# Kernel tuning notes

Measured on AMD Instinct MI355X. Metric: run time of the kernel, lower is better.

## Reference

```python
import jax, jax.numpy as jnp
import numpy as np

NEG_SLOPE = 0.1

def lrelu(x):
    return jnp.where(x >= 0, x, NEG_SLOPE * x)

def conv2d(x, w, b, padding=0, dilation=1):
    y = jax.lax.conv_general_dilated(
        x, w, window_strides=(1, 1),
        padding=[(padding, padding), (padding, padding)],
        rhs_dilation=(dilation, dilation),
        dimension_numbers=('NCHW', 'OIHW', 'NCHW'))
    return y + b[None, :, None, None]

def res_aspp(x, p):
    r1 = lrelu(conv2d(x, p['a1_w'], p['a1_b'], padding=1, dilation=1))
    r2 = lrelu(conv2d(x, p['a2_w'], p['a2_b'], padding=2, dilation=2))
    r3 = lrelu(conv2d(x, p['a3_w'], p['a3_b'], padding=4, dilation=4))
    r = conv2d(jnp.concatenate((r1, r2, r3), axis=1), p['ar_w'], p['ar_b'])
    return x + r

def deform_conv2d(x, offset, w, b):
    # x: [B,C,H,W], offset: [B,2*K,H,W] torchvision layout (y,x) per 3x3 tap
    B, C, H, W = x.shape
    KH = KW = 3
    K = KH * KW
    pad = 1
    off = offset.reshape(B, K, 2, H, W)
    ky, kx = jnp.meshgrid(jnp.arange(KH), jnp.arange(KW), indexing='ij')
    ky = ky.reshape(K).astype(x.dtype)
    kx = kx.reshape(K).astype(x.dtype)
    hh = jnp.arange(H, dtype=x.dtype)
    ww = jnp.arange(W, dtype=x.dtype)
    # sampling positions [B,K,H,W]
    py = off[:, :, 0] + (hh[None, None, :, None] - pad + ky[None, :, None, None])
    px = off[:, :, 1] + (ww[None, None, None, :] - pad + kx[None, :, None, None])
    y0 = jnp.floor(py)
    x0 = jnp.floor(px)
    wy = (py - y0)[:, None]  # [B,1,K,H,W]
    wx = (px - x0)[:, None]
    y0i = y0.astype(jnp.int32)
    x0i = x0.astype(jnp.int32)
    x_flat = x.reshape(B, C, H * W)

    def gather(iy, ix):
        valid = ((iy >= 0) & (iy < H) & (ix >= 0) & (ix < W)).astype(x.dtype)
        idx = jnp.clip(iy, 0, H - 1) * W + jnp.clip(ix, 0, W - 1)  # [B,K,H,W]
        v = jax.vmap(lambda xb, ib: xb[:, ib])(x_flat, idx.reshape(B, -1))
        return v.reshape(B, C, K, H, W) * valid[:, None]

    samp = (gather(y0i, x0i) * (1 - wy) * (1 - wx)
            + gather(y0i, x0i + 1) * (1 - wy) * wx
            + gather(y0i + 1, x0i) * wy * (1 - wx)
            + gather(y0i + 1, x0i + 1) * wy * wx)
    out = jnp.einsum('bckhw,ock->bohw', samp, w.reshape(w.shape[0], C, K))
    return out + b[None, :, None, None]

def setup_inputs() -> dict:
    key = jax.random.key(0)
    ks = jax.random.split(key, 16)
    B, C, H, W = 4, 64, 160, 160
    Cout = 64
    s = 0.05
    d = {
        'in_aux': jax.random.normal(ks[0], (B, C, H, W), jnp.float32),
        'in_ref': jax.random.normal(ks[1], (B, C, H, W), jnp.float32),
        'w01': jax.random.normal(ks[2], (Cout, 2 * C, 1, 1), jnp.float32) * s,
        'b01': jnp.zeros((Cout,), jnp.float32),
        'a1_w': jax.random.normal(ks[3], (Cout, Cout, 3, 3), jnp.float32) * s,
        'a1_b': jnp.zeros((Cout,), jnp.float32),
        'a2_w': jax.random.normal(ks[4], (Cout, Cout, 3, 3), jnp.float32) * s,
        'a2_b': jnp.zeros((Cout,), jnp.float32),
        'a3_w': jax.random.normal(ks[5], (Cout, Cout, 3, 3), jnp.float32) * s,
        'a3_b': jnp.zeros((Cout,), jnp.float32),
        'ar_w': jax.random.normal(ks[6], (Cout, 3 * Cout, 1, 1), jnp.float32) * s,
        'ar_b': jnp.zeros((Cout,), jnp.float32),
        'w02': jax.random.normal(ks[7], (18, Cout, 1, 1), jnp.float32) * s,
        'b02': jnp.zeros((18,), jnp.float32),
        'dw': jax.random.normal(ks[8], (Cout, C, 3, 3), jnp.float32) * s,
        'db': jnp.zeros((Cout,), jnp.float32),
    }
    return d

def reference(in_aux, in_ref, w01, b01, a1_w, a1_b, a2_w, a2_b, a3_w, a3_b,
              ar_w, ar_b, w02, b02, dw, db):
    cat_x = jnp.concatenate((in_aux, in_ref), axis=1)
    off_x = lrelu(conv2d(cat_x, w01, b01))
    p = {'a1_w': a1_w, 'a1_b': a1_b, 'a2_w': a2_w, 'a2_b': a2_b,
         'a3_w': a3_w, 'a3_b': a3_b, 'ar_w': ar_w, 'ar_b': ar_b}
    off_x = res_aspp(off_x, p)
    off_x = conv2d(off_x, w02, b02)
    return deform_conv2d(in_aux, off_x, dw, db)
```

## Files before the change

### kernel.cpp

```cpp
#include <hip/hip_runtime.h>
#include <math.h>

static constexpr int B = 4, H = 160, W = 160;
static constexpr int HW = H * W;
static constexpr int CHW = 64 * HW;
static constexpr int NELEM = B * CHW;

static constexpr int WP = 168;
static constexpr int HP = 168;
static constexpr int PHW = WP * HP;
static constexpr int PGUARD = 704;
static constexpr int PSTRIDE = 30720;
static constexpr int IMGOFS = PGUARD + 4 * WP + 4;

typedef short bf16x8 __attribute__((ext_vector_type(8)));
typedef float f32x4 __attribute__((ext_vector_type(4)));

__device__ __forceinline__ float lrelu(float v) { return v >= 0.f ? v : 0.1f * v; }

__device__ __forceinline__ unsigned short f2bf(float f) {
  unsigned u = __float_as_uint(f);
  return (unsigned short)((u + 0x7FFFu + ((u >> 16) & 1u)) >> 16);
}
__device__ __forceinline__ float bf2f(short u) {
  return __uint_as_float(((unsigned)(unsigned short)u) << 16);
}

__device__ __forceinline__ void glds16(const void* g, void* l) {
  __builtin_amdgcn_global_load_lds(
      (const __attribute__((address_space(1))) void*)g,
      (__attribute__((address_space(3))) void*)l, 16, 0, 0);
}

__global__ __launch_bounds__(256) void k_transform(
    const float* __restrict__ w01, const float* __restrict__ dw,
    const float* __restrict__ arw, const float* __restrict__ a1w,
    const float* __restrict__ a2w, const float* __restrict__ a3w,
    float* __restrict__ wt01, unsigned short* __restrict__ wb_bf,
    unsigned short* __restrict__ wd_bf, unsigned short* __restrict__ arw_bf,
    unsigned short* __restrict__ off0p) {
  int i = blockIdx.x * 256 + threadIdx.x;
  uint4* zp = (uint4*)off0p;
#pragma unroll
  for (int j = 0; j < 6; ++j) {
    unsigned u = (unsigned)i + (unsigned)j * 167936u;
    if (u < 983040u) zp[u] = make_uint4(0u, 0u, 0u, 0u);
  }
  if (i < 8192) {
    int ci = i >> 6, o = i & 63;
    wt01[i] = w01[o * 128 + ci];
  } else if (i < 118784) {
    int j = i - 8192;
    int ci = j & 63, co = (j >> 6) & 63;
    int kk = j >> 12;
    int dsel = kk / 9; kk -= dsel * 9;
    const float* src = dsel == 0 ? a1w : dsel == 1 ? a2w : a3w;
    wb_bf[j] = f2bf(src[(co * 64 + ci) * 9 + kk]);
  } else if (i < 155648) {
    int j = i - 118784;
    int ci = j & 63, co = (j >> 6) & 63, k = j >> 12;
    wd_bf[j] = f2bf(dw[(co * 64 + ci) * 9 + k]);
  } else if (i < 167936) {
    int j = i - 155648;
    arw_bf[j] = f2bf(arw[j]);
  }
}

__global__ __launch_bounds__(256) void k_conv1x1_in(
    const float* __restrict__ aux, const float* __restrict__ ref,
    const float* __restrict__ wt01, const float* __restrict__ b01,
    float* __restrict__ out, unsigned short* __restrict__ off0p,
    unsigned short* __restrict__ x_bf) {
  __shared__ float s[128 * 64];
  int pos0 = blockIdx.x * 64;
  int b = pos0 / HW;
  int hw0 = pos0 - b * HW;
  int tid = threadIdx.x;
  for (int i = tid; i < 8192; i += 256) {
    int ci = i >> 6, p = i & 63;
    const float* src = (ci < 64) ? (aux + b * CHW + ci * HW)
                                 : (ref + b * CHW + (ci - 64) * HW);
    s[i] = src[hw0 + p];
  }
  __syncthreads();
  int p = tid & 63;
  int g = __builtin_amdgcn_readfirstlane(tid >> 6);
  const float* wp = wt01 + g * 16;
  float acc[16];
#pragma unroll
  for (int j = 0; j < 16; ++j) acc[j] = 0.f;
#pragma unroll 4
  for (int ci = 0; ci < 128; ++ci) {
    float sv = s[ci * 64 + p];
    const float* wrow = wp + ci * 64;
#pragma unroll
    for (int j = 0; j < 16; ++j) acc[j] += sv * wrow[j];
  }
  const float* bb = b01 + g * 16;
  int obase = (b * 64 + g * 16) * HW + hw0 + p;
  unsigned short tb[16];
#pragma unroll
  for (int j = 0; j < 16; ++j) {
    float v = lrelu(acc[j] + bb[j]);
    out[obase + j * HW] = v;
    tb[j] = f2bf(v);
  }
  int hw = hw0 + p;
  int h = hw / W, w = hw - h * W;
  unsigned short* dst =
      off0p + ((size_t)b * PSTRIDE + IMGOFS + h * WP + w) * 64 + g * 16;
  *(uint4*)dst = *(const uint4*)&tb[0];
  *(uint4*)(dst + 8) = *(const uint4*)&tb[8];
  unsigned short xb[16];
#pragma unroll
  for (int j = 0; j < 16; ++j) xb[j] = f2bf(s[(g * 16 + j) * 64 + p]);
  unsigned short* xdst = x_bf + ((size_t)(b * HW + hw0 + p)) * 64 + g * 16;
  *(uint4*)xdst = *(const uint4*)&xb[0];
  *(uint4*)(xdst + 8) = *(const uint4*)&xb[8];
}

__global__ __launch_bounds__(256) void k_aspp3_mfma(
    const unsigned short* __restrict__ off0p,
    const unsigned short* __restrict__ wb_bf,
    const float* __restrict__ a1b, const float* __restrict__ a2b,
    const float* __restrict__ a3b, unsigned short* __restrict__ r_bf) {
  __shared__ unsigned short sa[2][288 * 64];
  int tid = threadIdx.x;
  int lane = tid & 63, wid = tid >> 6;
  int m = lane & 15, q = lane >> 4;

  int p0 = blockIdx.x;
  int xcd = p0 & 7, ii = p0 >> 3;
  int base = xcd < 4 ? xcd * 167 : 668 + (xcd - 4) * 166;
  int lid = base + ii;
  int dsel = lid % 3;
  int tj = lid / 3;
  int b = tj / 111;
  int tile = tj - b * 111;
  int pos0 = tile * 256;
  const int d = 1 << dsel;
  const unsigned short* pb = off0p + (size_t)b * PSTRIDE * 64;
  const float* bias = dsel == 0 ? a1b : dsel == 1 ? a2b : a3b;

  f32x4 acc[4][4] = {};

  auto STAGE = [&](int buf, int ky) {
    const char* src =
        (const char*)(pb + (size_t)(PGUARD + pos0 + (ky - 1) * d * WP - 16) * 64);
    char* dstb = (char*)&sa[buf][0];
#pragma unroll
    for (int r = 0; r < 9; ++r) {
      int X = r * 4096 + tid * 16;
      int row = X >> 7;
      int Xs = X ^ ((row & 7) << 4);
      glds16(src + Xs, dstb + X);
    }
  };
  auto COMPUTE = [&](int buf, int ky) {
    const char* sb = (const char*)&sa[buf][0];
#pragma unroll
    for (int kx = 0; kx < 3; ++kx) {
      const unsigned short* wk = wb_bf + (dsel * 9 + ky * 3 + kx) * 4096;
      int px0 = 16 + (kx - 1) * d + wid * 64;
#pragma unroll
      for (int kc = 0; kc < 2; ++kc) {
        bf16x8 bfrag[4];
#pragma unroll
        for (int t = 0; t < 4; ++t)
          bfrag[t] = *(const bf16x8*)(wk + (t * 16 + m) * 64 + kc * 32 + q * 8);
#pragma unroll
        for (int mt = 0; mt < 4; ++mt) {
          int px = px0 + mt * 16 + m;
          int byteoff = px * 128 + ((kc * 64 + q * 16) ^ ((px & 7) << 4));
          bf16x8 afrag = *(const bf16x8*)(sb + byteoff);
#pragma unroll
          for (int t = 0; t < 4; ++t)
            acc[mt][t] = __builtin_amdgcn_mfma_f32_16x16x32_bf16(
                afrag, bfrag[t], acc[mt][t], 0, 0, 0);
        }
      }
    }
  };

  STAGE(0, 0);
  __syncthreads();
  STAGE(1, 1);
  COMPUTE(0, 0);
  __syncthreads();
  STAGE(0, 2);
  COMPUTE(1, 1);
  __syncthreads();
  COMPUTE(0, 2);

  __syncthreads();
  unsigned short* epb = &sa[0][0];
#pragma unroll
  for (int t = 0; t < 4; ++t) {
    float bi = bias[t * 16 + m];
#pragma unroll
    for (int mt = 0; mt < 4; ++mt)
#pragma unroll
      for (int r = 0; r < 4; ++r)
        epb[(wid * 64 + mt * 16 + q * 4 + r) * 68 + t * 16 + m] =
            f2bf(lrelu(acc[mt][t][r] + bi));
  }
  __syncthreads();
  {
    int qa = pos0 + tid;
    int pr = qa / WP, pc = qa - pr * WP;
    if (pr >= 4 && pr < 164 && pc >= 4 && pc < 164) {
      int hw = (pr - 4) * W + (pc - 4);
      unsigned short* dst = r_bf + ((size_t)(b * HW + hw)) * 192 + dsel * 64;
      const unsigned short* s2 = epb + tid * 68;
#pragma unroll
      for (int c = 0; c < 8; ++c)
        *(uint4*)(dst + c * 8) = *(const uint4*)(s2 + c * 8);
    }
  }
}

__global__ __launch_bounds__(256) void k_merge_head_mfma(
    const unsigned short* __restrict__ r_bf, const float* __restrict__ off0,
    const unsigned short* __restrict__ arw_bf, const float* __restrict__ arb,
    const float* __restrict__ w02, const float* __restrict__ b02,
    float* __restrict__ offs) {
  __shared__ unsigned short sa[64 * 200];
  int pos0 = blockIdx.x * 64;
  int b = pos0 / HW;
  int hw0 = pos0 - b * HW;
  int tid = threadIdx.x;
  const unsigned short* gsrc = r_bf + (size_t)(b * HW + hw0) * 192;
  for (int i = tid; i < 1536; i += 256) {
    int pos = i / 24, c8 = i - pos * 24;
    *(uint4*)(sa + pos * 200 + c8 * 8) = *(const uint4*)(gsrc + i * 8);
  }
  __syncthreads();
  int lane = tid & 63, wid = tid >> 6;
  int m = lane & 15, q = lane >> 4;
  f32x4 acc[4] = {};
#pragma unroll
  for (int kc = 0; kc < 6; ++kc) {
    bf16x8 bfrag = *(const bf16x8*)(arw_bf + (wid * 16 + m) * 192 + kc * 32 + q * 8);
#pragma unroll
    for (int mt = 0; mt < 4; ++mt) {
      bf16x8 afrag = *(const bf16x8*)(sa + (mt * 16 + m) * 200 + kc * 32 + q * 8);
      acc[mt] = __builtin_amdgcn_mfma_f32_16x16x32_bf16(afrag, bfrag, acc[mt],
                                                        0, 0, 0);
    }
  }
  __syncthreads();
  float* ep = (float*)sa;
  int co = wid * 16 + m;
  float bi = arb[co];
  const float* resrow = off0 + (size_t)(b * 64 + co) * HW + hw0;
#pragma unroll
  for (int mt = 0; mt < 4; ++mt)
#pragma unroll
    for (int r = 0; r < 4; ++r) {
      int pos = mt * 16 + q * 4 + r;
      ep[pos * 65 + co] = acc[mt][r] + bi + resrow[pos];
    }
  __syncthreads();
  for (int i = tid; i < 1152; i += 256) {
    int t = i >> 6, p = i & 63;
    const float* w2 = w02 + t * 64;
    float o = b02[t];
#pragma unroll 8
    for (int c = 0; c < 64; ++c) o += ep[p * 65 + c] * w2[c];
    offs[(b * 18 + t) * HW + hw0 + p] = o;
  }
}

__global__ __launch_bounds__(256) void k_deform_mfma(
    const unsigned short* __restrict__ x_bf, const float* __restrict__ offs,
    const unsigned short* __restrict__ wd_bf, const float* __restrict__ db,
    float* __restrict__ out) {
  constexpr int SP = 72;
  __shared__ unsigned short sb[2][64 * SP];
  int blk = (blockIdx.x & 7) * 200 + (blockIdx.x >> 3);
  int pos0 = blk * 64;
  int b = pos0 / HW;
  int hw0 = pos0 - b * HW;
  int tid = threadIdx.x;
  int lane = tid & 63, wid = tid >> 6;
  int m = lane & 15, q = lane >> 4;
  int p = lane;
  int cg = wid;
  int hw = hw0 + p;
  int h = hw / W, wv = hw - h * W;
  const unsigned short* xb = x_bf + (size_t)b * HW * 64;
  const float* ob = offs + b * 18 * HW + hw;
  float offv[18];
#pragma unroll
  for (int j = 0; j < 18; ++j) offv[j] = ob[j * HW];
  f32x4 acc[4] = {};

#pragma unroll
  for (int k = 0; k < 9; ++k) {
    const int ky = k / 3, kx = k - ky * 3;
    float py = offv[2 * k] + (float)(h - 1 + ky);
    float px = offv[2 * k + 1] + (float)(wv - 1 + kx);
    float fy = floorf(py), fx = floorf(px);
    int iy0 = (int)fy, ix0 = (int)fx;
    float wy = py - fy, wx = px - fx;
    int iy1 = iy0 + 1, ix1 = ix0 + 1;
    float vy0 = (iy0 >= 0 && iy0 < H) ? 1.f : 0.f;
    float vy1 = (iy1 >= 0 && iy1 < H) ? 1.f : 0.f;
    float vx0 = (ix0 >= 0 && ix0 < W) ? 1.f : 0.f;
    float vx1 = (ix1 >= 0 && ix1 < W) ? 1.f : 0.f;
    int cy0 = min(max(iy0, 0), H - 1), cy1 = min(max(iy1, 0), H - 1);
    int cx0 = min(max(ix0, 0), W - 1), cx1 = min(max(ix1, 0), W - 1);
    float c00 = vy0 * vx0 * (1.f - wy) * (1.f - wx);
    float c01 = vy0 * vx1 * (1.f - wy) * wx;
    float c10 = vy1 * vx0 * wy * (1.f - wx);
    float c11 = vy1 * vx1 * wy * wx;
    const unsigned short* p00 = xb + (size_t)(cy0 * W + cx0) * 64 + cg * 16;
    const unsigned short* p01 = xb + (size_t)(cy0 * W + cx1) * 64 + cg * 16;
    const unsigned short* p10 = xb + (size_t)(cy1 * W + cx0) * 64 + cg * 16;
    const unsigned short* p11 = xb + (size_t)(cy1 * W + cx1) * 64 + cg * 16;
    unsigned short tb[16];
#pragma unroll
    for (int c2 = 0; c2 < 2; ++c2) {
      bf16x8 v00 = *(const bf16x8*)(p00 + c2 * 8);
      bf16x8 v01 = *(const bf16x8*)(p01 + c2 * 8);
      bf16x8 v10 = *(const bf16x8*)(p10 + c2 * 8);
      bf16x8 v11 = *(const bf16x8*)(p11 + c2 * 8);
#pragma unroll
      for (int j = 0; j < 8; ++j) {
        float sv = c00 * bf2f(v00[j]) + c01 * bf2f(v01[j]) +
                   c10 * bf2f(v10[j]) + c11 * bf2f(v11[j]);
        tb[c2 * 8 + j] = f2bf(sv);
      }
    }
    unsigned short* wr = &sb[k & 1][p * SP + cg * 16];
    *(uint4*)wr = *(const uint4*)&tb[0];
    *(uint4*)(wr + 8) = *(const uint4*)&tb[8];
    __syncthreads();
    const unsigned short* rb = &sb[k & 1][0];
#pragma unroll
    for (int kc = 0; kc < 2; ++kc) {
      bf16x8 bfrag =
          *(const bf16x8*)(wd_bf + (k * 64 + wid * 16 + m) * 64 + kc * 32 + q * 8);
#pragma unroll
      for (int mt = 0; mt < 4; ++mt) {
        bf16x8 afrag = *(const bf16x8*)(rb + (mt * 16 + m) * SP + kc * 32 + q * 8);
        acc[mt] = __builtin_amdgcn_mfma_f32_16x16x32_bf16(afrag, bfrag, acc[mt],
                                                          0, 0, 0);
      }
    }
  }
  int co = wid * 16 + m;
  float bias = db[co];
  size_t orow = (size_t)(b * 64 + co) * HW + hw0;
#pragma unroll
  for (int mt = 0; mt < 4; ++mt)
#pragma unroll
    for (int r = 0; r < 4; ++r)
      out[orow + mt * 16 + q * 4 + r] = acc[mt][r] + bias;
}

extern "C" void kernel_launch(void* const* d_in, const int* in_sizes, int n_in,
                              void* d_out, int out_size, void* d_ws, size_t ws_size,
                              hipStream_t stream) {
  const float* aux = (const float*)d_in[0];
  const float* ref = (const float*)d_in[1];
  const float* w01 = (const float*)d_in[2];
  const float* b01 = (const float*)d_in[3];
  const float* a1w = (const float*)d_in[4];
  const float* a1b = (const float*)d_in[5];
  const float* a2w = (const float*)d_in[6];
  const float* a2b = (const float*)d_in[7];
  const float* a3w = (const float*)d_in[8];
  const float* a3b = (const float*)d_in[9];
  const float* arw = (const float*)d_in[10];
  const float* arb = (const float*)d_in[11];
  const float* w02 = (const float*)d_in[12];
  const float* b02 = (const float*)d_in[13];
  const float* dw  = (const float*)d_in[14];
  const float* db  = (const float*)d_in[15];
  float* out = (float*)d_out;

  float* off0 = (float*)d_ws;
  float* offs = off0 + NELEM;
  float* wt01 = offs + B * 18 * HW;
  unsigned short* off0p = (unsigned short*)(wt01 + 8192);
  unsigned short* x_bf   = off0p + (size_t)B * PSTRIDE * 64;
  unsigned short* wb_bf  = x_bf + (size_t)NELEM;
  unsigned short* wd_bf  = wb_bf + 110592;
  unsigned short* arw_bf = wd_bf + 36864;
  unsigned short* r_bf   = arw_bf + 12288;

  k_transform<<<656, 256, 0, stream>>>(w01, dw, arw, a1w, a2w, a3w,
                                       wt01, wb_bf, wd_bf, arw_bf, off0p);
  k_conv1x1_in<<<B * HW / 64, 256, 0, stream>>>(aux, ref, wt01, b01, off0,
                                                off0p, x_bf);
  k_aspp3_mfma<<<1332, 256, 0, stream>>>(off0p, wb_bf, a1b, a2b, a3b, r_bf);
  k_merge_head_mfma<<<B * HW / 64, 256, 0, stream>>>(
      r_bf, off0, arw_bf, arb, w02, b02, offs);
  k_deform_mfma<<<B * HW / 64, 256, 0, stream>>>(x_bf, offs, wd_bf, db, out);
}
```

Baseline: 328.9 us.

## Build deform-conv MFMA A-fragments in registers, dropping LDS staging and barriers

```diff
diff --git a/kernel.cpp b/kernel.cpp
--- a/kernel.cpp
+++ b/kernel.cpp
@@ -275,8 +275,6 @@
     const unsigned short* __restrict__ x_bf, const float* __restrict__ offs,
     const unsigned short* __restrict__ wd_bf, const float* __restrict__ db,
     float* __restrict__ out) {
-  constexpr int SP = 72;
-  __shared__ unsigned short sb[2][64 * SP];
   int blk = (blockIdx.x & 7) * 200 + (blockIdx.x >> 3);
   int pos0 = blk * 64;
   int b = pos0 / HW;
@@ -284,9 +282,7 @@
   int tid = threadIdx.x;
   int lane = tid & 63, wid = tid >> 6;
   int m = lane & 15, q = lane >> 4;
-  int p = lane;
-  int cg = wid;
-  int hw = hw0 + p;
+  int hw = hw0 + wid * 16 + m;
   int h = hw / W, wv = hw - h * W;
   const unsigned short* xb = x_bf + (size_t)b * HW * 64;
   const float* ob = offs + b * 18 * HW + hw;
@@ -314,49 +310,45 @@
     float c01 = vy0 * vx1 * (1.f - wy) * wx;
     float c10 = vy1 * vx0 * wy * (1.f - wx);
     float c11 = vy1 * vx1 * wy * wx;
-    const unsigned short* p00 = xb + (size_t)(cy0 * W + cx0) * 64 + cg * 16;
-    const unsigned short* p01 = xb + (size_t)(cy0 * W + cx1) * 64 + cg * 16;
-    const unsigned short* p10 = xb + (size_t)(cy1 * W + cx0) * 64 + cg * 16;
-    const unsigned short* p11 = xb + (size_t)(cy1 * W + cx1) * 64 + cg * 16;
-    unsigned short tb[16];
-#pragma unroll
-    for (int c2 = 0; c2 < 2; ++c2) {
-      bf16x8 v00 = *(const bf16x8*)(p00 + c2 * 8);
-      bf16x8 v01 = *(const bf16x8*)(p01 + c2 * 8);
-      bf16x8 v10 = *(const bf16x8*)(p10 + c2 * 8);
-      bf16x8 v11 = *(const bf16x8*)(p11 + c2 * 8);
+    const unsigned short* p00 = xb + (size_t)(cy0 * W + cx0) * 64 + q * 8;
+    const unsigned short* p01 = xb + (size_t)(cy0 * W + cx1) * 64 + q * 8;
+    const unsigned short* p10 = xb + (size_t)(cy1 * W + cx0) * 64 + q * 8;
+    const unsigned short* p11 = xb + (size_t)(cy1 * W + cx1) * 64 + q * 8;
+    bf16x8 afrag[2];
+#pragma unroll
+    for (int kc = 0; kc < 2; ++kc) {
+      bf16x8 v00 = *(const bf16x8*)(p00 + kc * 32);
+      bf16x8 v01 = *(const bf16x8*)(p01 + kc * 32);
+      bf16x8 v10 = *(const bf16x8*)(p10 + kc * 32);
+      bf16x8 v11 = *(const bf16x8*)(p11 + kc * 32);
+      unsigned short tb[8];
 #pragma unroll
       for (int j = 0; j < 8; ++j) {
         float sv = c00 * bf2f(v00[j]) + c01 * bf2f(v01[j]) +
                    c10 * bf2f(v10[j]) + c11 * bf2f(v11[j]);
-        tb[c2 * 8 + j] = f2bf(sv);
+        tb[j] = f2bf(sv);
       }
-    }
-    unsigned short* wr = &sb[k & 1][p * SP + cg * 16];
-    *(uint4*)wr = *(const uint4*)&tb[0];
-    *(uint4*)(wr + 8) = *(const uint4*)&tb[8];
-    __syncthreads();
-    const unsigned short* rb = &sb[k & 1][0];
-#pragma unroll
-    for (int kc = 0; kc < 2; ++kc) {
-      bf16x8 bfrag =
-          *(const bf16x8*)(wd_bf + (k * 64 + wid * 16 + m) * 64 + kc * 32 + q * 8);
-#pragma unroll
-      for (int mt = 0; mt < 4; ++mt) {
-        bf16x8 afrag = *(const bf16x8*)(rb + (mt * 16 + m) * SP + kc * 32 + q * 8);
-        acc[mt] = __builtin_amdgcn_mfma_f32_16x16x32_bf16(afrag, bfrag, acc[mt],
-                                                          0, 0, 0);
+      afrag[kc] = *(const bf16x8*)&tb[0];
+    }
+#pragma unroll
+    for (int kc = 0; kc < 2; ++kc)
+#pragma unroll
+      for (int t = 0; t < 4; ++t) {
+        bf16x8 bfrag = *(const bf16x8*)(wd_bf + (k * 64 + t * 16 + m) * 64 +
+                                        kc * 32 + q * 8);
+        acc[t] = __builtin_amdgcn_mfma_f32_16x16x32_bf16(afrag[kc], bfrag,
+                                                         acc[t], 0, 0, 0);
       }
-    }
-  }
-  int co = wid * 16 + m;
-  float bias = db[co];
-  size_t orow = (size_t)(b * 64 + co) * HW + hw0;
-#pragma unroll
-  for (int mt = 0; mt < 4; ++mt)
+  }
+#pragma unroll
+  for (int t = 0; t < 4; ++t) {
+    int co = t * 16 + m;
+    float bias = db[co];
+    size_t orow = (size_t)(b * 64 + co) * HW + hw0 + wid * 16;
 #pragma unroll
     for (int r = 0; r < 4; ++r)
-      out[orow + mt * 16 + q * 4 + r] = acc[mt][r] + bias;
+      out[orow + q * 4 + r] = acc[t][r] + bias;
+  }
 }
 
 extern "C" void kernel_launch(void* const* d_in, const int* in_sizes, int n_in,
```

After: 362.1 us. 1.1x slower.

## Prefetch next tap's bilinear gathers and XOR-swizzle deform LDS tile

Applied to the files above, without the earlier changes.

```diff
diff --git a/kernel.cpp b/kernel.cpp
--- a/kernel.cpp
+++ b/kernel.cpp
@@ -275,8 +275,7 @@
     const unsigned short* __restrict__ x_bf, const float* __restrict__ offs,
     const unsigned short* __restrict__ wd_bf, const float* __restrict__ db,
     float* __restrict__ out) {
-  constexpr int SP = 72;
-  __shared__ unsigned short sb[2][64 * SP];
+  __shared__ unsigned short sb[2][64 * 64];
   int blk = (blockIdx.x & 7) * 200 + (blockIdx.x >> 3);
   int pos0 = blk * 64;
   int b = pos0 / HW;
@@ -295,8 +294,10 @@
   for (int j = 0; j < 18; ++j) offv[j] = ob[j * HW];
   f32x4 acc[4] = {};
 
-#pragma unroll
-  for (int k = 0; k < 9; ++k) {
+  bf16x8 va[8], vb[8];
+  float ca[4], cb[4];
+
+  auto PREP = [&](int k, bf16x8* v, float* c) {
     const int ky = k / 3, kx = k - ky * 3;
     float py = offv[2 * k] + (float)(h - 1 + ky);
     float px = offv[2 * k + 1] + (float)(wv - 1 + kx);
@@ -310,40 +311,52 @@
     float vx1 = (ix1 >= 0 && ix1 < W) ? 1.f : 0.f;
     int cy0 = min(max(iy0, 0), H - 1), cy1 = min(max(iy1, 0), H - 1);
     int cx0 = min(max(ix0, 0), W - 1), cx1 = min(max(ix1, 0), W - 1);
-    float c00 = vy0 * vx0 * (1.f - wy) * (1.f - wx);
-    float c01 = vy0 * vx1 * (1.f - wy) * wx;
-    float c10 = vy1 * vx0 * wy * (1.f - wx);
-    float c11 = vy1 * vx1 * wy * wx;
+    c[0] = vy0 * vx0 * (1.f - wy) * (1.f - wx);
+    c[1] = vy0 * vx1 * (1.f - wy) * wx;
+    c[2] = vy1 * vx0 * wy * (1.f - wx);
+    c[3] = vy1 * vx1 * wy * wx;
     const unsigned short* p00 = xb + (size_t)(cy0 * W + cx0) * 64 + cg * 16;
     const unsigned short* p01 = xb + (size_t)(cy0 * W + cx1) * 64 + cg * 16;
     const unsigned short* p10 = xb + (size_t)(cy1 * W + cx0) * 64 + cg * 16;
     const unsigned short* p11 = xb + (size_t)(cy1 * W + cx1) * 64 + cg * 16;
+    v[0] = *(const bf16x8*)(p00);  v[1] = *(const bf16x8*)(p00 + 8);
+    v[2] = *(const bf16x8*)(p01);  v[3] = *(const bf16x8*)(p01 + 8);
+    v[4] = *(const bf16x8*)(p10);  v[5] = *(const bf16x8*)(p10 + 8);
+    v[6] = *(const bf16x8*)(p11);  v[7] = *(const bf16x8*)(p11 + 8);
+  };
+
+  PREP(0, va, ca);
+#pragma unroll
+  for (int k = 0; k < 9; ++k) {
+    bf16x8* vc = (k & 1) ? vb : va;
+    float* cc = (k & 1) ? cb : ca;
+    bf16x8* vn = (k & 1) ? va : vb;
+    float* cn = (k & 1) ? ca : cb;
+    if (k < 8) PREP(k + 1, vn, cn);
+
     unsigned short tb[16];
 #pragma unroll
-    for (int c2 = 0; c2 < 2; ++c2) {
-      bf16x8 v00 = *(const bf16x8*)(p00 + c2 * 8);
-      bf16x8 v01 = *(const bf16x8*)(p01 + c2 * 8);
-      bf16x8 v10 = *(const bf16x8*)(p10 + c2 * 8);
-      bf16x8 v11 = *(const bf16x8*)(p11 + c2 * 8);
+    for (int half = 0; half < 2; ++half)
 #pragma unroll
       for (int j = 0; j < 8; ++j) {
-        float sv = c00 * bf2f(v00[j]) + c01 * bf2f(v01[j]) +
-                   c10 * bf2f(v10[j]) + c11 * bf2f(v11[j]);
-        tb[c2 * 8 + j] = f2bf(sv);
+        float sv = cc[0] * bf2f(vc[0 + half][j]) + cc[1] * bf2f(vc[2 + half][j]) +
+                   cc[2] * bf2f(vc[4 + half][j]) + cc[3] * bf2f(vc[6 + half][j]);
+        tb[half * 8 + j] = f2bf(sv);
       }
-    }
-    unsigned short* wr = &sb[k & 1][p * SP + cg * 16];
-    *(uint4*)wr = *(const uint4*)&tb[0];
-    *(uint4*)(wr + 8) = *(const uint4*)&tb[8];
+    char* base = (char*)&sb[k & 1][p * 64];
+    *(uint4*)(base + ((cg * 32) ^ ((p & 7) << 4))) = *(const uint4*)&tb[0];
+    *(uint4*)(base + ((cg * 32 + 16) ^ ((p & 7) << 4))) = *(const uint4*)&tb[8];
     __syncthreads();
-    const unsigned short* rb = &sb[k & 1][0];
+    const char* rb = (const char*)&sb[k & 1][0];
 #pragma unroll
     for (int kc = 0; kc < 2; ++kc) {
       bf16x8 bfrag =
           *(const bf16x8*)(wd_bf + (k * 64 + wid * 16 + m) * 64 + kc * 32 + q * 8);
 #pragma unroll
       for (int mt = 0; mt < 4; ++mt) {
-        bf16x8 afrag = *(const bf16x8*)(rb + (mt * 16 + m) * SP + kc * 32 + q * 8);
+        int row = mt * 16 + m;
+        int off = (kc * 64 + q * 16) ^ ((row & 7) << 4);
+        bf16x8 afrag = *(const bf16x8*)(rb + row * 128 + off);
         acc[mt] = __builtin_amdgcn_mfma_f32_16x16x32_bf16(afrag, bfrag, acc[mt],
                                                           0, 0, 0);
       }
```

Measured after the change: 326.0 us. No clear change (-0.9%).

## Software-pipeline deform gather loads one tap ahead with swizzled LDS and packed bf16 convert

Applied to the files above, without the earlier changes.

```diff
diff --git a/kernel.cpp b/kernel.cpp
--- a/kernel.cpp
+++ b/kernel.cpp
@@ -271,12 +271,81 @@
   }
 }
 
+#define DEF_SET(S) \
+  bf16x8 S##v0, S##v1, S##v2, S##v3, S##v4, S##v5, S##v6, S##v7; \
+  float S##c0, S##c1, S##c2, S##c3;
+
+#define PREP(kk, S) do { \
+    const int ky = (kk) / 3, kx = (kk) - ky * 3; \
+    float py = offv[2 * (kk)] + (float)(h - 1 + ky); \
+    float px = offv[2 * (kk) + 1] + (float)(wv - 1 + kx); \
+    float fy = floorf(py), fx = floorf(px); \
+    int iy0 = (int)fy, ix0 = (int)fx; \
+    float wy = py - fy, wx = px - fx; \
+    int iy1 = iy0 + 1, ix1 = ix0 + 1; \
+    float vy0 = (iy0 >= 0 && iy0 < H) ? 1.f : 0.f; \
+    float vy1 = (iy1 >= 0 && iy1 < H) ? 1.f : 0.f; \
+    float vx0 = (ix0 >= 0 && ix0 < W) ? 1.f : 0.f; \
+    float vx1 = (ix1 >= 0 && ix1 < W) ? 1.f : 0.f; \
+    int cy0 = min(max(iy0, 0), H - 1), cy1 = min(max(iy1, 0), H - 1); \
+    int cx0 = min(max(ix0, 0), W - 1), cx1 = min(max(ix1, 0), W - 1); \
+    S##c0 = vy0 * vx0 * (1.f - wy) * (1.f - wx); \
+    S##c1 = vy0 * vx1 * (1.f - wy) * wx; \
+    S##c2 = vy1 * vx0 * wy * (1.f - wx); \
+    S##c3 = vy1 * vx1 * wy * wx; \
+    const unsigned short* q00 = xbase + (size_t)(cy0 * W + cx0) * 64 + cg * 16; \
+    const unsigned short* q01 = xbase + (size_t)(cy0 * W + cx1) * 64 + cg * 16; \
+    const unsigned short* q10 = xbase + (size_t)(cy1 * W + cx0) * 64 + cg * 16; \
+    const unsigned short* q11 = xbase + (size_t)(cy1 * W + cx1) * 64 + cg * 16; \
+    S##v0 = *(const bf16x8*)(q00); S##v1 = *(const bf16x8*)(q00 + 8); \
+    S##v2 = *(const bf16x8*)(q01); S##v3 = *(const bf16x8*)(q01 + 8); \
+    S##v4 = *(const bf16x8*)(q10); S##v5 = *(const bf16x8*)(q10 + 8); \
+    S##v6 = *(const bf16x8*)(q11); S##v7 = *(const bf16x8*)(q11 + 8); \
+  } while (0)
+
+#define CONSUME(kk, S) do { \
+    unsigned tw0[4], tw1[4]; \
+    _Pragma("unroll") \
+    for (int jj = 0; jj < 4; ++jj) { \
+      float s0 = S##c0 * bf2f(S##v0[2 * jj]) + S##c1 * bf2f(S##v2[2 * jj]) + \
+                 S##c2 * bf2f(S##v4[2 * jj]) + S##c3 * bf2f(S##v6[2 * jj]); \
+      float s1 = S##c0 * bf2f(S##v0[2 * jj + 1]) + S##c1 * bf2f(S##v2[2 * jj + 1]) + \
+                 S##c2 * bf2f(S##v4[2 * jj + 1]) + S##c3 * bf2f(S##v6[2 * jj + 1]); \
+      asm("v_cvt_pk_bf16_f32 %0, %1, %2" : "=v"(tw0[jj]) : "v"(s0), "v"(s1)); \
+      float s2 = S##c0 * bf2f(S##v1[2 * jj]) + S##c1 * bf2f(S##v3[2 * jj]) + \
+                 S##c2 * bf2f(S##v5[2 * jj]) + S##c3 * bf2f(S##v7[2 * jj]); \
+      float s3 = S##c0 * bf2f(S##v1[2 * jj + 1]) + S##c1 * bf2f(S##v3[2 * jj + 1]) + \
+                 S##c2 * bf2f(S##v5[2 * jj + 1]) + S##c3 * bf2f(S##v7[2 * jj + 1]); \
+      asm("v_cvt_pk_bf16_f32 %0, %1, %2" : "=v"(tw1[jj]) : "v"(s2), "v"(s3)); \
+    } \
+    char* basep = (char*)&sb[(kk) & 1][(size_t)p * 64]; \
+    *(uint4*)(basep + ((cg * 32) ^ ((p & 7) << 4))) = *(const uint4*)&tw0[0]; \
+    *(uint4*)(basep + ((cg * 32 + 16) ^ ((p & 7) << 4))) = *(const uint4*)&tw1[0]; \
+    __builtin_amdgcn_sched_barrier(0); \
+    asm volatile("s_waitcnt lgkmcnt(0)" ::: "memory"); \
+    __builtin_amdgcn_s_barrier(); \
+    __builtin_amdgcn_sched_barrier(0); \
+    const char* rbp = (const char*)&sb[(kk) & 1][0]; \
+    _Pragma("unroll") \
+    for (int kc = 0; kc < 2; ++kc) { \
+      bf16x8 bfrag = *(const bf16x8*)(wd_bf + ((kk) * 64 + wid * 16 + m) * 64 + \
+                                      kc * 32 + q * 8); \
+      _Pragma("unroll") \
+      for (int mt = 0; mt < 4; ++mt) { \
+        int row = mt * 16 + m; \
+        int off = (kc * 64 + q * 16) ^ ((row & 7) << 4); \
+        bf16x8 afrag = *(const bf16x8*)(rbp + row * 128 + off); \
+        acc[mt] = __builtin_amdgcn_mfma_f32_16x16x32_bf16(afrag, bfrag, acc[mt], \
+                                                          0, 0, 0); \
+      } \
+    } \
+  } while (0)
+
 __global__ __launch_bounds__(256) void k_deform_mfma(
     const unsigned short* __restrict__ x_bf, const float* __restrict__ offs,
     const unsigned short* __restrict__ wd_bf, const float* __restrict__ db,
     float* __restrict__ out) {
-  constexpr int SP = 72;
-  __shared__ unsigned short sb[2][64 * SP];
+  __shared__ unsigned short sb[2][64 * 64];
   int blk = (blockIdx.x & 7) * 200 + (blockIdx.x >> 3);
   int pos0 = blk * 64;
   int b = pos0 / HW;
@@ -288,67 +357,26 @@
   int cg = wid;
   int hw = hw0 + p;
   int h = hw / W, wv = hw - h * W;
-  const unsigned short* xb = x_bf + (size_t)b * HW * 64;
+  const unsigned short* xbase = x_bf + (size_t)b * HW * 64;
   const float* ob = offs + b * 18 * HW + hw;
   float offv[18];
 #pragma unroll
   for (int j = 0; j < 18; ++j) offv[j] = ob[j * HW];
   f32x4 acc[4] = {};
 
-#pragma unroll
-  for (int k = 0; k < 9; ++k) {
-    const int ky = k / 3, kx = k - ky * 3;
-    float py = offv[2 * k] + (float)(h - 1 + ky);
-    float px = offv[2 * k + 1] + (float)(wv - 1 + kx);
-    float fy = floorf(py), fx = floorf(px);
-    int iy0 = (int)fy, ix0 = (int)fx;
-    float wy = py - fy, wx = px - fx;
-    int iy1 = iy0 + 1, ix1 = ix0 + 1;
-    float vy0 = (iy0 >= 0 && iy0 < H) ? 1.f : 0.f;
-    float vy1 = (iy1 >= 0 && iy1 < H) ? 1.f : 0.f;
-    float vx0 = (ix0 >= 0 && ix0 < W) ? 1.f : 0.f;
-    float vx1 = (ix1 >= 0 && ix1 < W) ? 1.f : 0.f;
-    int cy0 = min(max(iy0, 0), H - 1), cy1 = min(max(iy1, 0), H - 1);
-    int cx0 = min(max(ix0, 0), W - 1), cx1 = min(max(ix1, 0), W - 1);
-    float c00 = vy0 * vx0 * (1.f - wy) * (1.f - wx);
-    float c01 = vy0 * vx1 * (1.f - wy) * wx;
-    float c10 = vy1 * vx0 * wy * (1.f - wx);
-    float c11 = vy1 * vx1 * wy * wx;
-    const unsigned short* p00 = xb + (size_t)(cy0 * W + cx0) * 64 + cg * 16;
-    const unsigned short* p01 = xb + (size_t)(cy0 * W + cx1) * 64 + cg * 16;
-    const unsigned short* p10 = xb + (size_t)(cy1 * W + cx0) * 64 + cg * 16;
-    const unsigned short* p11 = xb + (size_t)(cy1 * W + cx1) * 64 + cg * 16;
-    unsigned short tb[16];
-#pragma unroll
-    for (int c2 = 0; c2 < 2; ++c2) {
-      bf16x8 v00 = *(const bf16x8*)(p00 + c2 * 8);
-      bf16x8 v01 = *(const bf16x8*)(p01 + c2 * 8);
-      bf16x8 v10 = *(const bf16x8*)(p10 + c2 * 8);
-      bf16x8 v11 = *(const bf16x8*)(p11 + c2 * 8);
-#pragma unroll
-      for (int j = 0; j < 8; ++j) {
-        float sv = c00 * bf2f(v00[j]) + c01 * bf2f(v01[j]) +
-                   c10 * bf2f(v10[j]) + c11 * bf2f(v11[j]);
-        tb[c2 * 8 + j] = f2bf(sv);
-      }
-    }
-    unsigned short* wr = &sb[k & 1][p * SP + cg * 16];
-    *(uint4*)wr = *(const uint4*)&tb[0];
-    *(uint4*)(wr + 8) = *(const uint4*)&tb[8];
-    __syncthreads();
-    const unsigned short* rb = &sb[k & 1][0];
-#pragma unroll
-    for (int kc = 0; kc < 2; ++kc) {
-      bf16x8 bfrag =
-          *(const bf16x8*)(wd_bf + (k * 64 + wid * 16 + m) * 64 + kc * 32 + q * 8);
-#pragma unroll
-      for (int mt = 0; mt < 4; ++mt) {
-        bf16x8 afrag = *(const bf16x8*)(rb + (mt * 16 + m) * SP + kc * 32 + q * 8);
-        acc[mt] = __builtin_amdgcn_mfma_f32_16x16x32_bf16(afrag, bfrag, acc[mt],
-                                                          0, 0, 0);
-      }
-    }
-  }
+  DEF_SET(A) DEF_SET(B)
+
+  PREP(0, A);
+  PREP(1, B); __builtin_amdgcn_sched_barrier(0); CONSUME(0, A);
+  PREP(2, A); __builtin_amdgcn_sched_barrier(0); CONSUME(1, B);
+  PREP(3, B); __builtin_amdgcn_sched_barrier(0); CONSUME(2, A);
+  PREP(4, A); __builtin_amdgcn_sched_barrier(0); CONSUME(3, B);
+  PREP(5, B); __builtin_amdgcn_sched_barrier(0); CONSUME(4, A);
+  PREP(6, A); __builtin_amdgcn_sched_barrier(0); CONSUME(5, B);
+  PREP(7, B); __builtin_amdgcn_sched_barrier(0); CONSUME(6, A);
+  PREP(8, A); __builtin_amdgcn_sched_barrier(0); CONSUME(7, B);
+  CONSUME(8, A);
+
   int co = wid * 16 + m;
   float bias = db[co];
   size_t orow = (size_t)(b * 64 + co) * HW + hw0;
```

After: 326.0 us. Within noise of the previous version (-0.9%).
